# Optimization experiments

Measured on AMD Instinct MI355X. Metric: run time of the kernel, lower is better.

Reference implementation:

```python
import jax, jax.numpy as jnp
from jax import lax
import numpy as np

B = 32        # graphs per batch
NN = 513      # nodes per graph (odd M so Y/Z head lengths match)
IN = 128      # input_dim
OUT = 256     # output_dim
T = 4         # edge_types
STEPS = 4     # ggnn propagation steps
DEG = 16
N = B * NN
E = N * DEG
CAT = IN + OUT


def setup_inputs() -> dict:
    key = jax.random.key(0)
    ks = jax.random.split(key, 16)
    f32 = jnp.float32
    feature = jax.random.normal(ks[0], (N, IN), f32)
    offs = (jnp.arange(B) * NN)[:, None]
    edge_src = (jax.random.randint(ks[1], (B, NN * DEG), 0, NN) + offs).reshape(-1)
    edge_dst = (jax.random.randint(ks[2], (B, NN * DEG), 0, NN) + offs).reshape(-1)
    edge_type = jax.random.randint(ks[3], (E,), 0, T)
    s = 1.0 / np.sqrt(OUT)
    W_msg = jax.random.normal(ks[4], (T, OUT, OUT), f32) * s      # [T, out, in] (torch Linear layout)
    b_msg = jnp.zeros((T, OUT), f32)
    gru_w_ih = jax.random.normal(ks[5], (3 * OUT, OUT), f32) * s
    gru_w_hh = jax.random.normal(ks[6], (3 * OUT, OUT), f32) * s
    gru_b_ih = jnp.zeros((3 * OUT,), f32)
    gru_b_hh = jnp.zeros((3 * OUT,), f32)
    conv1_w = jax.random.normal(ks[7], (OUT, OUT, 3), f32) * (1.0 / np.sqrt(OUT * 3))
    conv1_b = jnp.zeros((OUT,), f32)
    conv2_w = jax.random.normal(ks[8], (OUT, OUT, 1), f32) * s
    conv2_b = jnp.zeros((OUT,), f32)
    convc1_w = jax.random.normal(ks[9], (CAT, CAT, 3), f32) * (1.0 / np.sqrt(CAT * 3))
    convc1_b = jnp.zeros((CAT,), f32)
    convc2_w = jax.random.normal(ks[10], (CAT, CAT, 2), f32) * (1.0 / np.sqrt(CAT * 2))
    convc2_b = jnp.zeros((CAT,), f32)
    mlpy_w = jax.random.normal(ks[11], (1, OUT), f32) * s
    mlpy_b = jnp.zeros((1,), f32)
    mlpz_w = jax.random.normal(ks[12], (1, CAT), f32) * (1.0 / np.sqrt(CAT))
    mlpz_b = jnp.zeros((1,), f32)
    return dict(feature=feature, W_msg=W_msg, b_msg=b_msg,
                gru_w_ih=gru_w_ih, gru_w_hh=gru_w_hh, gru_b_ih=gru_b_ih, gru_b_hh=gru_b_hh,
                conv1_w=conv1_w, conv1_b=conv1_b, conv2_w=conv2_w, conv2_b=conv2_b,
                convc1_w=convc1_w, convc1_b=convc1_b, convc2_w=convc2_w, convc2_b=convc2_b,
                mlpy_w=mlpy_w, mlpy_b=mlpy_b, mlpz_w=mlpz_w, mlpz_b=mlpz_b,
                edge_src=edge_src, edge_dst=edge_dst, edge_type=edge_type)


def _conv1d(x, w, b):
    # x: [B, C_in, L], w: [C_out, C_in, K]
    y = lax.conv_general_dilated(x, w, (1,), 'VALID', dimension_numbers=('NCH', 'OIH', 'NCH'))
    return y + b[None, :, None]


def _maxpool1d(x, k, s):
    init = jnp.array(-jnp.inf, dtype=x.dtype)
    return lax.reduce_window(x, init, lax.max, (1, 1, k), (1, 1, s), 'VALID')


def _forward(feature, W_msg, b_msg, gru_w_ih, gru_w_hh, gru_b_ih, gru_b_hh,
             conv1_w, conv1_b, conv2_w, conv2_b, convc1_w, convc1_b, convc2_w, convc2_b,
             mlpy_w, mlpy_b, mlpz_w, mlpz_b, edge_src, edge_dst, edge_type):
    # --- GatedGraphConv (DGL semantics): zero-pad features to out_feats ---
    h = jnp.pad(feature, ((0, 0), (0, OUT - IN)))  # [N, OUT]
    for _ in range(STEPS):
        # per-etype linear on all nodes: hw[t] = h @ W_msg[t].T + b_msg[t]
        hw = jnp.einsum('nd,tod->tno', h, W_msg) + b_msg[:, None, :]   # [T, N, OUT]
        msg = hw[edge_type, edge_src]                                   # [E, OUT] gather
        a = jax.ops.segment_sum(msg, edge_dst, num_segments=N)          # [N, OUT] scatter-add
        # GRUCell(a, h) in torch gate order (r, z, n)
        gi = a @ gru_w_ih.T + gru_b_ih
        gh = h @ gru_w_hh.T + gru_b_hh
        ir, iz, inn = jnp.split(gi, 3, axis=-1)
        hr, hz, hn = jnp.split(gh, 3, axis=-1)
        r = jax.nn.sigmoid(ir + hr)
        z = jax.nn.sigmoid(iz + hz)
        n = jnp.tanh(inn + r * hn)
        h = (1.0 - z) * n + z * h
    outputs = h                                             # [N, OUT]
    ci = jnp.concatenate([outputs, feature], axis=-1)       # [N, OUT+IN]
    # batchify to [B, C, L]
    hi = outputs.reshape(B, NN, OUT).transpose(0, 2, 1)
    cb = ci.reshape(B, NN, CAT).transpose(0, 2, 1)
    Y1 = _maxpool1d(jax.nn.relu(_conv1d(hi, conv1_w, conv1_b)), 3, 2)
    Y2 = _maxpool1d(jax.nn.relu(_conv1d(Y1, conv2_w, conv2_b)), 2, 2).transpose(0, 2, 1)   # [B, 127, OUT]
    Z1 = _maxpool1d(jax.nn.relu(_conv1d(cb, convc1_w, convc1_b)), 3, 2)
    Z2 = _maxpool1d(jax.nn.relu(_conv1d(Z1, convc2_w, convc2_b)), 2, 2).transpose(0, 2, 1)  # [B, 127, CAT]
    before_avg = (Y2 @ mlpy_w.T + mlpy_b) * (Z2 @ mlpz_w.T + mlpz_b)   # [B, 127, 1]
    avg = before_avg.mean(axis=1)                                       # [B, 1]
    return jax.nn.sigmoid(avg).squeeze(-1)                              # [B]


def reference(feature, W_msg, b_msg, gru_w_ih, gru_w_hh, gru_b_ih, gru_b_hh,
              conv1_w, conv1_b, conv2_w, conv2_b, convc1_w, convc1_b, convc2_w, convc2_b,
              mlpy_w, mlpy_b, mlpz_w, mlpz_b, edge_src, edge_dst, edge_type):
    return _forward(feature, W_msg, b_msg, gru_w_ih, gru_w_hh, gru_b_ih, gru_b_hh,
                    conv1_w, conv1_b, conv2_w, conv2_b, convc1_w, convc1_b, convc2_w, convc2_b,
                    mlpy_w, mlpy_b, mlpz_w, mlpz_b, edge_src, edge_dst, edge_type)
```

## Files before the change

kernel.cpp:

```cpp
#include <hip/hip_runtime.h>

#define Bg    32
#define NNg   513
#define INF   128
#define OUTF  256
#define TT    4
#define NSTEP 4
#define DEGg  16
#define Ntot  (Bg*NNg)
#define Etot  (Ntot*DEGg)
#define CATF  (OUTF+INF)
#define SK    1056
#define NB    (Ntot*TT)
#define NSB2  129

typedef _Float16 h8_t __attribute__((ext_vector_type(8)));
typedef _Float16 h4_t __attribute__((ext_vector_type(4)));
typedef float    f4_t __attribute__((ext_vector_type(4)));

__global__ void pad_h_k(const float* __restrict__ feat, float* __restrict__ h,
                        _Float16* __restrict__ h16) {
  int idx = blockIdx.x*256 + threadIdx.x;
  if (idx >= Ntot*OUTF) return;
  int n = idx >> 8, c = idx & 255;
  float v = (c < INF) ? feat[n*INF + c] : 0.f;
  h[idx] = v;
  h16[idx] = (_Float16)v;
}

__global__ void cvt_k(const float* __restrict__ s, _Float16* __restrict__ d, int n) {
  int i = (blockIdx.x*256 + threadIdx.x) * 4;
  if (i >= n) return;
  float4 v = *reinterpret_cast<const float4*>(s + i);
  _Float16 o[4] = {(_Float16)v.x, (_Float16)v.y, (_Float16)v.z, (_Float16)v.w};
  *reinterpret_cast<ushort4*>(d + i) = *reinterpret_cast<ushort4*>(o);
}

__global__ void build_cb16_k(const _Float16* __restrict__ h16,
                             const float* __restrict__ feat,
                             _Float16* __restrict__ cb) {
  int idx = blockIdx.x*256 + threadIdx.x;
  if (idx >= Ntot*CATF) return;
  int n = idx / CATF, c = idx % CATF;
  cb[idx] = (c < OUTF) ? h16[n*OUTF + c] : (_Float16)feat[n*INF + (c - OUTF)];
}

__global__ void zero_int_k(int* __restrict__ p, int n) {
  int i = blockIdx.x*256 + threadIdx.x;
  if (i < n) p[i] = 0;
}

__global__ void hist_k(const int* __restrict__ dst, const int* __restrict__ typ,
                       int* __restrict__ cnt) {
  int e = blockIdx.x*256 + threadIdx.x;
  if (e < Etot) atomicAdd(&cnt[dst[e]*TT + typ[e]], 1);
}

__global__ void scan1_k(const int* __restrict__ cnt, int* __restrict__ rp2,
                        int* __restrict__ bsum) {
  __shared__ int buf[512];
  int t = threadIdx.x;
  int i = blockIdx.x*512 + t;
  int v = (i < NB) ? cnt[i] : 0;
  buf[t] = v;
  __syncthreads();
  #pragma unroll
  for (int off = 1; off < 512; off <<= 1) {
    int x = (t >= off) ? buf[t - off] : 0;
    __syncthreads();
    buf[t] += x;
    __syncthreads();
  }
  if (i < NB) rp2[i] = buf[t] - v;
  if (t == 511) bsum[blockIdx.x] = buf[511];
}

__global__ void scan2_k(int* __restrict__ bsum) {
  __shared__ int buf[256];
  int t = threadIdx.x;
  int v = (t < NSB2) ? bsum[t] : 0;
  buf[t] = v;
  __syncthreads();
  #pragma unroll
  for (int off = 1; off < 256; off <<= 1) {
    int x = (t >= off) ? buf[t - off] : 0;
    __syncthreads();
    buf[t] += x;
    __syncthreads();
  }
  if (t < NSB2) bsum[t] = buf[t] - v;
}

__global__ void scan3_k(int* __restrict__ rp2, const int* __restrict__ bsum) {
  int i = blockIdx.x*512 + threadIdx.x;
  if (i < NB) rp2[i] += bsum[blockIdx.x];
  if (i == 0) rp2[NB] = Etot;
}

__global__ void fill_k(const int* __restrict__ dst, const int* __restrict__ typ,
                       const int* __restrict__ src, const int* __restrict__ rp2,
                       int* __restrict__ cursor, int* __restrict__ srcv) {
  int e = blockIdx.x*256 + threadIdx.x;
  if (e < Etot) {
    int b = dst[e]*TT + typ[e];
    int pos = atomicAdd(&cursor[b], 1);
    srcv[rp2[b] + pos] = src[e];
  }
}

__global__ void gather_k(const _Float16* __restrict__ h16, const int* __restrict__ rp2,
                         const int* __restrict__ srcv, _Float16* __restrict__ s16) {
  __shared__ int src_s[128];
  int n = blockIdx.x;
  int c = threadIdx.x;
  int b0 = rp2[TT*n], e1 = rp2[TT*n+1], e2 = rp2[TT*n+2], e3 = rp2[TT*n+3], e4 = rp2[TT*n+4];
  float a0 = 0.f, a1 = 0.f, a2 = 0.f, a3 = 0.f;
  for (int base = b0; base < e4; base += 128) {
    int m = e4 - base; if (m > 128) m = 128;
    if (c < m) src_s[c] = srcv[base + c];
    __syncthreads();
    int s1 = min(max(e1 - base, 0), m);
    int s2 = min(max(e2 - base, 0), m);
    int s3 = min(max(e3 - base, 0), m);
#define SEG(ACC, ST, EN)                                                   \
    {                                                                      \
      int i = (ST);                                                        \
      for (; i + 4 <= (EN); i += 4) {                                      \
        float v0 = (float)h16[(size_t)src_s[i]  *256 + c];                 \
        float v1 = (float)h16[(size_t)src_s[i+1]*256 + c];                 \
        float v2 = (float)h16[(size_t)src_s[i+2]*256 + c];                 \
        float v3 = (float)h16[(size_t)src_s[i+3]*256 + c];                 \
        ACC += (v0 + v1) + (v2 + v3);                                      \
      }                                                                    \
      for (; i < (EN); ++i) ACC += (float)h16[(size_t)src_s[i]*256 + c];   \
    }
    SEG(a0, 0,  s1)
    SEG(a1, s1, s2)
    SEG(a2, s2, s3)
    SEG(a3, s3, m)
#undef SEG
    __syncthreads();
  }
  size_t b = (size_t)n * SK;
  s16[b + 0*256 + c] = (_Float16)a0;
  s16[b + 1*256 + c] = (_Float16)a1;
  s16[b + 2*256 + c] = (_Float16)a2;
  s16[b + 3*256 + c] = (_Float16)a3;
  if (c < 32) {
    int cv = (c == 0) ? (e1-b0) : (c == 1) ? (e2-e1) : (c == 2) ? (e3-e2) : (c == 3) ? (e4-e3) : 0;
    s16[b + 1024 + c] = (_Float16)(float)cv;
  }
}

__global__ void repack_wext_k(const float* __restrict__ Wmsg, const float* __restrict__ bmsg,
                              _Float16* __restrict__ wext) {
  int idx = blockIdx.x*256 + threadIdx.x;
  if (idx >= 256*SK) return;
  int co = idx / SK, k = idx % SK;
  float v;
  if (k < 1024)      { int t = k >> 8, ci = k & 255; v = Wmsg[((size_t)t*256 + co)*256 + ci]; }
  else if (k < 1028) { v = bmsg[(k - 1024)*256 + co]; }
  else               { v = 0.f; }
  wext[idx] = (_Float16)v;
}

__global__ void gru_gate_k(const _Float16* __restrict__ gi, const _Float16* __restrict__ gh,
                           float* __restrict__ h, _Float16* __restrict__ h16) {
  int idx = blockIdx.x*256 + threadIdx.x;
  if (idx >= Ntot*64) return;
  int n = idx >> 6, g4 = (idx & 63) * 4;
  const _Float16* gin = gi + (size_t)n*768 + g4;
  const _Float16* ghn = gh + (size_t)n*768 + g4;
  h4_t ir = *reinterpret_cast<const h4_t*>(gin);
  h4_t iz = *reinterpret_cast<const h4_t*>(gin + 256);
  h4_t in_ = *reinterpret_cast<const h4_t*>(gin + 512);
  h4_t hr = *reinterpret_cast<const h4_t*>(ghn);
  h4_t hz = *reinterpret_cast<const h4_t*>(ghn + 256);
  h4_t hn = *reinterpret_cast<const h4_t*>(ghn + 512);
  size_t hb = (size_t)n*256 + g4;
  float4 hv = *reinterpret_cast<const float4*>(h + hb);
  float hvv[4] = {hv.x, hv.y, hv.z, hv.w};
  float ov[4];
  _Float16 ov16[4];
  #pragma unroll
  for (int j = 0; j < 4; ++j) {
    float r  = 1.f / (1.f + expf(-((float)ir[j] + (float)hr[j])));
    float z  = 1.f / (1.f + expf(-((float)iz[j] + (float)hz[j])));
    float nn = tanhf((float)in_[j] + r * (float)hn[j]);
    float o = (1.f - z) * nn + z * hvv[j];
    ov[j] = o;
    ov16[j] = (_Float16)o;
  }
  float4 os = {ov[0], ov[1], ov[2], ov[3]};
  *reinterpret_cast<float4*>(h + hb) = os;
  *reinterpret_cast<ushort4*>(h16 + hb) = *reinterpret_cast<ushort4*>(ov16);
}

template<typename IT, typename OT>
__global__ void maxpool_k(const IT* __restrict__ in, OT* __restrict__ out,
                          int Lin, int Lp, int C, int kwin) {
  int idx = blockIdx.x*256 + threadIdx.x;
  int total = Bg*Lp*C;
  if (idx >= total) return;
  int c = idx % C; int r = idx / C; int p = r % Lp; int b = r / Lp;
  const IT* base = in + ((size_t)(b*Lin + 2*p))*C + c;
  float v = (float)base[0];
  for (int w = 1; w < kwin; ++w) v = fmaxf(v, (float)base[(size_t)w*C]);
  out[idx] = (OT)v;
}

__global__ void repack16_k(const float* __restrict__ w, _Float16* __restrict__ wk,
                           int Cout, int Cin, int K) {
  int idx = blockIdx.x*256 + threadIdx.x;
  int total = Cout*Cin*K;
  if (idx >= total) return;
  int ci = idx % Cin; int r = idx / Cin; int k = r % K; int co = r / K;
  wk[idx] = (_Float16)w[(co*Cin + ci)*K + k];
}

__global__ void head_k(const float* __restrict__ Y2, const float* __restrict__ Z2,
                       const float* __restrict__ wy, const float* __restrict__ by,
                       const float* __restrict__ wz, const float* __restrict__ bz,
                       float* __restrict__ out) {
  int b = blockIdx.x;
  int tid = threadIdx.x;
  __shared__ float red[128];
  float sum = 0.f;
  for (int p = tid; p < 127; p += 128) {
    const float* yr = Y2 + ((size_t)(b*127 + p))*OUTF;
    const float* zr = Z2 + ((size_t)(b*127 + p))*CATF;
    float yv = by[0], zv = bz[0];
    for (int c = 0; c < OUTF; ++c) yv = fmaf(yr[c], wy[c], yv);
    for (int c = 0; c < CATF; ++c) zv = fmaf(zr[c], wz[c], zv);
    sum += yv * zv;
  }
  red[tid] = sum;
  __syncthreads();
  for (int off = 64; off > 0; off >>= 1) {
    if (tid < off) red[tid] += red[tid + off];
    __syncthreads();
  }
  if (tid == 0) out[b] = 1.f / (1.f + expf(-red[0] / 127.f));
}

template<typename CT, bool RELU, bool MAPPED>
__global__ __launch_bounds__(256, 2) void hgemm(
    const _Float16* __restrict__ A, const _Float16* __restrict__ W,
    const float* __restrict__ bias, CT* __restrict__ C,
    int M, int Nout, int K, int arstride, int Lout, int NNodes) {
  __shared__ _Float16 As[128][40];
  __shared__ _Float16 Ws[128][40];
  int tid = threadIdx.x;
  int lane = tid & 63, wid = tid >> 6;
  int wm = wid >> 1, wn = wid & 1;
  int l15 = lane & 15, l4 = lane >> 4;
  int m0 = blockIdx.x * 128, n0 = blockIdx.y * 128;

  int s_row = tid >> 1;
  int s_col = (tid & 1) * 16;
  int m_s = m0 + s_row;
  bool a_ok = (m_s < M);
  int mc = a_ok ? m_s : (M - 1);
  int node = MAPPED ? (mc / Lout) * NNodes + (mc % Lout) : mc;
  const _Float16* a_src = A + (size_t)node * arstride + s_col;
  const _Float16* w_src = W + (size_t)(n0 + s_row) * K + s_col;

  f4_t acc[4][4] = {};

  for (int k0 = 0; k0 < K; k0 += 32) {
    if (k0) __syncthreads();
    int4 va0 = {0,0,0,0}, va1 = {0,0,0,0};
    if (a_ok) {
      const int4* ga = reinterpret_cast<const int4*>(a_src + k0);
      va0 = ga[0]; va1 = ga[1];
    }
    const int4* gw = reinterpret_cast<const int4*>(w_src + k0);
    int4 vw0 = gw[0], vw1 = gw[1];
    *reinterpret_cast<int4*>(&As[s_row][s_col])     = va0;
    *reinterpret_cast<int4*>(&As[s_row][s_col + 8]) = va1;
    *reinterpret_cast<int4*>(&Ws[s_row][s_col])     = vw0;
    *reinterpret_cast<int4*>(&Ws[s_row][s_col + 8]) = vw1;
    __syncthreads();

    h8_t af[4], bf[4];
    #pragma unroll
    for (int fm = 0; fm < 4; ++fm)
      af[fm] = *reinterpret_cast<const h8_t*>(&As[wm*64 + fm*16 + l15][l4*8]);
    #pragma unroll
    for (int fn = 0; fn < 4; ++fn)
      bf[fn] = *reinterpret_cast<const h8_t*>(&Ws[wn*64 + fn*16 + l15][l4*8]);
    #pragma unroll
    for (int fm = 0; fm < 4; ++fm)
      #pragma unroll
      for (int fn = 0; fn < 4; ++fn)
        acc[fm][fn] = __builtin_amdgcn_mfma_f32_16x16x32_f16(af[fm], bf[fn], acc[fm][fn], 0, 0, 0);
  }

  #pragma unroll
  for (int fn = 0; fn < 4; ++fn) {
    int col = n0 + wn*64 + fn*16 + l15;
    float bv = bias[col];
    #pragma unroll
    for (int fm = 0; fm < 4; ++fm) {
      #pragma unroll
      for (int i = 0; i < 4; ++i) {
        int m = m0 + wm*64 + fm*16 + l4*4 + i;
        if (m >= M) continue;
        float v = acc[fm][fn][i] + bv;
        if (RELU) v = fmaxf(v, 0.f);
        C[(size_t)m * Nout + col] = (CT)v;
      }
    }
  }
}

static inline int cdiv(int x, int y) { return (x + y - 1) / y; }

extern "C" void kernel_launch(void* const* d_in, const int* in_sizes, int n_in,
                              void* d_out, int out_size, void* d_ws, size_t ws_size,
                              hipStream_t stream) {
  const float* feature  = (const float*)d_in[0];
  const float* W_msg    = (const float*)d_in[1];
  const float* b_msg    = (const float*)d_in[2];
  const float* w_ih     = (const float*)d_in[3];
  const float* w_hh     = (const float*)d_in[4];
  const float* b_ih     = (const float*)d_in[5];
  const float* b_hh     = (const float*)d_in[6];
  const float* conv1_w  = (const float*)d_in[7];
  const float* conv1_b  = (const float*)d_in[8];
  const float* conv2_w  = (const float*)d_in[9];
  const float* conv2_b  = (const float*)d_in[10];
  const float* convc1_w = (const float*)d_in[11];
  const float* convc1_b = (const float*)d_in[12];
  const float* convc2_w = (const float*)d_in[13];
  const float* convc2_b = (const float*)d_in[14];
  const float* mlpy_w   = (const float*)d_in[15];
  const float* mlpy_b   = (const float*)d_in[16];
  const float* mlpz_w   = (const float*)d_in[17];
  const float* mlpz_b   = (const float*)d_in[18];
  const int*   esrc     = (const int*)d_in[19];
  const int*   edst     = (const int*)d_in[20];
  const int*   etyp     = (const int*)d_in[21];
  float* out = (float*)d_out;

  char* base = (char*)d_ws;
  size_t off = 0;
  auto alloc = [&](size_t bytes) { void* p = base + off; off = (off + bytes + 255) & ~(size_t)255; return p; };
  float*    h      = (float*)   alloc((size_t)Ntot*OUTF*4);
  _Float16* h16    = (_Float16*)alloc((size_t)Ntot*OUTF*2);
  _Float16* Wext16 = (_Float16*)alloc((size_t)256*SK*2);
  _Float16* wih16  = (_Float16*)alloc((size_t)768*256*2);
  _Float16* whh16  = (_Float16*)alloc((size_t)768*256*2);
  float*    bias0  = (float*)   alloc(256*4);
  int* rp2    = (int*)alloc((NB+1)*4);
  int* cnt    = (int*)alloc(NB*4);
  int* bsum   = (int*)alloc(NSB2*4);
  int* srcv   = (int*)alloc((size_t)Etot*4);
  char* big   = (char*)alloc((size_t)Ntot*1536*4);
  _Float16* gi  = (_Float16*)big;
  _Float16* gh  = gi + (size_t)Ntot*768;
  _Float16* s16 = (_Float16*)(big + (size_t)Ntot*768*4);
  _Float16* a16 = s16 + (size_t)Ntot*SK;
  float*    Y2   = (float*)big;
  float*    Z2   = Y2 + (size_t)Bg*127*OUTF;
  _Float16* y1   = (_Float16*)(Z2 + (size_t)Bg*127*CATF);
  float*    y2   = (float*)(y1 + (size_t)Bg*511*OUTF);
  _Float16* p1   = (_Float16*)(y2 + (size_t)Bg*255*OUTF);
  _Float16* cb16 = p1 + (size_t)Bg*255*OUTF;
  _Float16* z1   = cb16 + (size_t)Ntot*CATF;
  float*    z2   = (float*)(z1 + (size_t)Bg*511*CATF);
  _Float16* pz1  = (_Float16*)(z2 + (size_t)Bg*254*CATF);
  _Float16* wk1  = pz1 + (size_t)Bg*255*CATF;
  _Float16* wkc1 = wk1 + (size_t)256*768;
  _Float16* wkc2 = wkc1 + (size_t)384*1152;
  _Float16* c2w16= wkc2 + (size_t)384*768;

  dim3 blk(256);

  pad_h_k<<<cdiv(Ntot*OUTF,256), blk, 0, stream>>>(feature, h, h16);
  repack_wext_k<<<cdiv(256*SK,256), blk, 0, stream>>>(W_msg, b_msg, Wext16);
  cvt_k<<<cdiv(768*256/4,256), blk, 0, stream>>>(w_ih, wih16, 768*256);
  cvt_k<<<cdiv(768*256/4,256), blk, 0, stream>>>(w_hh, whh16, 768*256);
  hipMemsetAsync(bias0, 0, 256*4, stream);

  zero_int_k<<<cdiv(NB,256), blk, 0, stream>>>(cnt, NB);
  hist_k<<<cdiv(Etot,256), blk, 0, stream>>>(edst, etyp, cnt);
  scan1_k<<<NSB2, 512, 0, stream>>>(cnt, rp2, bsum);
  scan2_k<<<1, blk, 0, stream>>>(bsum);
  scan3_k<<<NSB2, 512, 0, stream>>>(rp2, bsum);
  zero_int_k<<<cdiv(NB,256), blk, 0, stream>>>(cnt, NB);
  fill_k<<<cdiv(Etot,256), blk, 0, stream>>>(edst, etyp, esrc, rp2, cnt, srcv);

  for (int s = 0; s < NSTEP; ++s) {
    gather_k<<<Ntot, blk, 0, stream>>>(h16, rp2, srcv, s16);
    hgemm<_Float16,false,false><<<dim3(cdiv(Ntot,128), 2), blk, 0, stream>>>(
        s16, Wext16, bias0, a16, Ntot, 256, SK, SK, 0, 0);
    hgemm<_Float16,false,false><<<dim3(cdiv(Ntot,128), 6), blk, 0, stream>>>(
        a16, wih16, b_ih, gi, Ntot, 768, 256, 256, 0, 0);
    hgemm<_Float16,false,false><<<dim3(cdiv(Ntot,128), 6), blk, 0, stream>>>(
        h16, whh16, b_hh, gh, Ntot, 768, 256, 256, 0, 0);
    gru_gate_k<<<cdiv(Ntot*64,256), blk, 0, stream>>>(gi, gh, h, h16);
  }

  repack16_k<<<cdiv(256*256*3,256), blk, 0, stream>>>(conv1_w,  wk1,  256, 256, 3);
  repack16_k<<<cdiv(384*384*3,256), blk, 0, stream>>>(convc1_w, wkc1, 384, 384, 3);
  repack16_k<<<cdiv(384*384*2,256), blk, 0, stream>>>(convc2_w, wkc2, 384, 384, 2);
  cvt_k<<<cdiv(256*256/4,256), blk, 0, stream>>>(conv2_w, c2w16, 256*256);

  hgemm<_Float16,true,true><<<dim3(cdiv(Bg*511,128), 2), blk, 0, stream>>>(
      h16, wk1, conv1_b, y1, Bg*511, 256, 768, 256, 511, NNg);
  maxpool_k<_Float16,_Float16><<<cdiv(Bg*255*256,256), blk, 0, stream>>>(y1, p1, 511, 255, 256, 3);
  hgemm<float,true,false><<<dim3(cdiv(Bg*255,128), 2), blk, 0, stream>>>(
      p1, c2w16, conv2_b, y2, Bg*255, 256, 256, 256, 0, 0);
  maxpool_k<float,float><<<cdiv(Bg*127*256,256), blk, 0, stream>>>(y2, Y2, 255, 127, 256, 2);

  build_cb16_k<<<cdiv(Ntot*CATF,256), blk, 0, stream>>>(h16, feature, cb16);
  hgemm<_Float16,true,true><<<dim3(cdiv(Bg*511,128), 3), blk, 0, stream>>>(
      cb16, wkc1, convc1_b, z1, Bg*511, 384, 1152, 384, 511, NNg);
  maxpool_k<_Float16,_Float16><<<cdiv(Bg*255*384,256), blk, 0, stream>>>(z1, pz1, 511, 255, 384, 3);
  hgemm<float,true,true><<<dim3(cdiv(Bg*254,128), 3), blk, 0, stream>>>(
      pz1, wkc2, convc2_b, z2, Bg*254, 384, 768, 384, 254, 255);
  maxpool_k<float,float><<<cdiv(Bg*127*384,256), blk, 0, stream>>>(z2, Z2, 254, 127, 384, 2);

  head_k<<<Bg, 128, 0, stream>>>(Y2, Z2, mlpy_w, mlpy_b, mlpz_w, mlpz_b, out);
}
```

Before: 877.5 us.

## Load GEMM tiles via global_load_lds with XOR swizzle and fuse GRU GEMMs

The hgemm kernel now moves A and W tiles straight from global memory into LDS with global_load_lds, instead of staging them through registers. It replaces the padded shared layout with an XOR-swizzled one to avoid bank conflicts. The two GRU input/hidden GEMMs are merged into one launch using a z-dimension that selects the operand set, and occupancy is raised to 3 blocks per SU. Out-of-range rows are now clamped and loaded rather than zero-filled, which relies on the epilogue masking those rows. The direct-to-LDS lane layout also depends on strict wave-ordering assumptions.

```diff
diff --git a/kernel.cpp b/kernel.cpp
--- a/kernel.cpp
+++ b/kernel.cpp
@@ -17,6 +17,11 @@
 typedef _Float16 h8_t __attribute__((ext_vector_type(8)));
 typedef _Float16 h4_t __attribute__((ext_vector_type(4)));
 typedef float    f4_t __attribute__((ext_vector_type(4)));
+
+#define GLL(gsrc, ldst)                                                        \
+  __builtin_amdgcn_global_load_lds(                                            \
+      (const __attribute__((address_space(1))) unsigned int*)(gsrc),           \
+      (__attribute__((address_space(3))) unsigned int*)(ldst), 16, 0, 0)
 
 __global__ void pad_h_k(const float* __restrict__ feat, float* __restrict__ h,
                         _Float16* __restrict__ h16) {
@@ -243,52 +248,55 @@
   if (tid == 0) out[b] = 1.f / (1.f + expf(-red[0] / 127.f));
 }
 
-template<typename CT, bool RELU, bool MAPPED>
-__global__ __launch_bounds__(256, 2) void hgemm(
+template<typename CT, bool RELU, bool MAPPED, bool DUAL>
+__global__ __launch_bounds__(256, 3) void hgemm(
     const _Float16* __restrict__ A, const _Float16* __restrict__ W,
     const float* __restrict__ bias, CT* __restrict__ C,
-    int M, int Nout, int K, int arstride, int Lout, int NNodes) {
-  __shared__ _Float16 As[128][40];
-  __shared__ _Float16 Ws[128][40];
+    int M, int Nout, int K, int arstride, int Lout, int NNodes,
+    const _Float16* A2, const _Float16* W2, const float* bias2, CT* C2) {
+  __shared__ _Float16 As[128*32];
+  __shared__ _Float16 Ws[128*32];
+  if (DUAL && blockIdx.z == 1) { A = A2; W = W2; bias = bias2; C = C2; }
   int tid = threadIdx.x;
   int lane = tid & 63, wid = tid >> 6;
   int wm = wid >> 1, wn = wid & 1;
   int l15 = lane & 15, l4 = lane >> 4;
   int m0 = blockIdx.x * 128, n0 = blockIdx.y * 128;
 
-  int s_row = tid >> 1;
-  int s_col = (tid & 1) * 16;
-  int m_s = m0 + s_row;
-  bool a_ok = (m_s < M);
-  int mc = a_ok ? m_s : (M - 1);
-  int node = MAPPED ? (mc / Lout) * NNodes + (mc % Lout) : mc;
-  const _Float16* a_src = A + (size_t)node * arstride + s_col;
-  const _Float16* w_src = W + (size_t)(n0 + s_row) * K + s_col;
-
+  int sr  = wid*16 + (lane >> 2);
+  int scol = ((lane & 3) ^ (sr & 3)) * 8;
+  int am0r = m0 + sr, am1r = m0 + sr + 64;
+  int am0 = (am0r < M) ? am0r : M - 1;
+  int am1 = (am1r < M) ? am1r : M - 1;
+  int an0 = MAPPED ? (am0 / Lout) * NNodes + (am0 % Lout) : am0;
+  int an1 = MAPPED ? (am1 / Lout) * NNodes + (am1 % Lout) : am1;
+  const _Float16* asrc0 = A + (size_t)an0 * arstride + scol;
+  const _Float16* asrc1 = A + (size_t)an1 * arstride + scol;
+  const _Float16* wsrc0 = W + (size_t)(n0 + sr) * K + scol;
+  const _Float16* wsrc1 = W + (size_t)(n0 + sr + 64) * K + scol;
+  _Float16* ald0 = As + (wid*16) * 32;
+  _Float16* ald1 = As + (64 + wid*16) * 32;
+  _Float16* wld0 = Ws + (wid*16) * 32;
+  _Float16* wld1 = Ws + (64 + wid*16) * 32;
+
+  int sl = l4 ^ (l15 & 3);
   f4_t acc[4][4] = {};
 
   for (int k0 = 0; k0 < K; k0 += 32) {
     if (k0) __syncthreads();
-    int4 va0 = {0,0,0,0}, va1 = {0,0,0,0};
-    if (a_ok) {
-      const int4* ga = reinterpret_cast<const int4*>(a_src + k0);
-      va0 = ga[0]; va1 = ga[1];
-    }
-    const int4* gw = reinterpret_cast<const int4*>(w_src + k0);
-    int4 vw0 = gw[0], vw1 = gw[1];
-    *reinterpret_cast<int4*>(&As[s_row][s_col])     = va0;
-    *reinterpret_cast<int4*>(&As[s_row][s_col + 8]) = va1;
-    *reinterpret_cast<int4*>(&Ws[s_row][s_col])     = vw0;
-    *reinterpret_cast<int4*>(&Ws[s_row][s_col + 8]) = vw1;
+    GLL(asrc0 + k0, ald0);
+    GLL(asrc1 + k0, ald1);
+    GLL(wsrc0 + k0, wld0);
+    GLL(wsrc1 + k0, wld1);
     __syncthreads();
 
     h8_t af[4], bf[4];
     #pragma unroll
     for (int fm = 0; fm < 4; ++fm)
-      af[fm] = *reinterpret_cast<const h8_t*>(&As[wm*64 + fm*16 + l15][l4*8]);
+      af[fm] = *reinterpret_cast<const h8_t*>(As + (wm*64 + fm*16 + l15)*32 + sl*8);
     #pragma unroll
     for (int fn = 0; fn < 4; ++fn)
-      bf[fn] = *reinterpret_cast<const h8_t*>(&Ws[wn*64 + fn*16 + l15][l4*8]);
+      bf[fn] = *reinterpret_cast<const h8_t*>(Ws + (wn*64 + fn*16 + l15)*32 + sl*8);
     #pragma unroll
     for (int fm = 0; fm < 4; ++fm)
       #pragma unroll
@@ -393,12 +401,12 @@
 
   for (int s = 0; s < NSTEP; ++s) {
     gather_k<<<Ntot, blk, 0, stream>>>(h16, rp2, srcv, s16);
-    hgemm<_Float16,false,false><<<dim3(cdiv(Ntot,128), 2), blk, 0, stream>>>(
-        s16, Wext16, bias0, a16, Ntot, 256, SK, SK, 0, 0);
-    hgemm<_Float16,false,false><<<dim3(cdiv(Ntot,128), 6), blk, 0, stream>>>(
-        a16, wih16, b_ih, gi, Ntot, 768, 256, 256, 0, 0);
-    hgemm<_Float16,false,false><<<dim3(cdiv(Ntot,128), 6), blk, 0, stream>>>(
-        h16, whh16, b_hh, gh, Ntot, 768, 256, 256, 0, 0);
+    hgemm<_Float16,false,false,false><<<dim3(cdiv(Ntot,128), 2), blk, 0, stream>>>(
+        s16, Wext16, bias0, a16, Ntot, 256, SK, SK, 0, 0,
+        nullptr, nullptr, nullptr, nullptr);
+    hgemm<_Float16,false,false,true><<<dim3(cdiv(Ntot,128), 6, 2), blk, 0, stream>>>(
+        a16, wih16, b_ih, gi, Ntot, 768, 256, 256, 0, 0,
+        h16, whh16, b_hh, gh);
     gru_gate_k<<<cdiv(Ntot*64,256), blk, 0, stream>>>(gi, gh, h, h16);
   }
 
@@ -407,19 +415,23 @@
   repack16_k<<<cdiv(384*384*2,256), blk, 0, stream>>>(convc2_w, wkc2, 384, 384, 2);
   cvt_k<<<cdiv(256*256/4,256), blk, 0, stream>>>(conv2_w, c2w16, 256*256);
 
-  hgemm<_Float16,true,true><<<dim3(cdiv(Bg*511,128), 2), blk, 0, stream>>>(
-      h16, wk1, conv1_b, y1, Bg*511, 256, 768, 256, 511, NNg);
+  hgemm<_Float16,true,true,false><<<dim3(cdiv(Bg*511,128), 2), blk, 0, stream>>>(
+      h16, wk1, conv1_b, y1, Bg*511, 256, 768, 256, 511, NNg,
+      nullptr, nullptr, nullptr, nullptr);
   maxpool_k<_Float16,_Float16><<<cdiv(Bg*255*256,256), blk, 0, stream>>>(y1, p1, 511, 255, 256, 3);
-  hgemm<float,true,false><<<dim3(cdiv(Bg*255,128), 2), blk, 0, stream>>>(
-      p1, c2w16, conv2_b, y2, Bg*255, 256, 256, 256, 0, 0);
+  hgemm<float,true,false,false><<<dim3(cdiv(Bg*255,128), 2), blk, 0, stream>>>(
+      p1, c2w16, conv2_b, y2, Bg*255, 256, 256, 256, 0, 0,
+      nullptr, nullptr, nullptr, nullptr);
   maxpool_k<float,float><<<cdiv(Bg*127*256,256), blk, 0, stream>>>(y2, Y2, 255, 127, 256, 2);
 
   build_cb16_k<<<cdiv(Ntot*CATF,256), blk, 0, stream>>>(h16, feature, cb16);
-  hgemm<_Float16,true,true><<<dim3(cdiv(Bg*511,128), 3), blk, 0, stream>>>(
-      cb16, wkc1, convc1_b, z1, Bg*511, 384, 1152, 384, 511, NNg);
+  hgemm<_Float16,true,true,false><<<dim3(cdiv(Bg*511,128), 3), blk, 0, stream>>>(
+      cb16, wkc1, convc1_b, z1, Bg*511, 384, 1152, 384, 511, NNg,
+      nullptr, nullptr, nullptr, nullptr);
   maxpool_k<_Float16,_Float16><<<cdiv(Bg*255*384,256), blk, 0, stream>>>(z1, pz1, 511, 255, 384, 3);
-  hgemm<float,true,true><<<dim3(cdiv(Bg*254,128), 3), blk, 0, stream>>>(
-      pz1, wkc2, convc2_b, z2, Bg*254, 384, 768, 384, 254, 255);
+  hgemm<float,true,true,false><<<dim3(cdiv(Bg*254,128), 3), blk, 0, stream>>>(
+      pz1, wkc2, convc2_b, z2, Bg*254, 384, 768, 384, 254, 255,
+      nullptr, nullptr, nullptr, nullptr);
   maxpool_k<float,float><<<cdiv(Bg*127*384,256), blk, 0, stream>>>(z2, Z2, 254, 127, 384, 2);
 
   head_k<<<Bg, 128, 0, stream>>>(Y2, Z2, mlpy_w, mlpy_b, mlpz_w, mlpz_b, out);
```

Measured after the change: 846.6 us. 1.04x faster.
